# Optimization experiments

Measured on AMD Instinct MI355X. Metric: run time of the kernel, lower is better.

The kernel has to match this reference:

```python
import jax, jax.numpy as jnp
import numpy as np

GROUP_SIZE = 128  # vLLM machete default group size
ZERO_POINT = 8.0  # uint4b8: stored unsigned 4-bit, logical value = q - 8


def setup_inputs() -> dict:
    key = jax.random.key(0)
    k_a, k_b, k_s = jax.random.split(key, 3)
    M, K, N = 4096, 4096, 12288
    a = jax.random.normal(k_a, (M, K), dtype=jnp.float32)
    # int4 quantized weights stored as small ints in [0, 16)
    b_q = jax.random.randint(k_b, (K, N), 0, 16, dtype=jnp.int32)
    # per-group scales: one scale per (group of 128 rows of K) per output column
    scales = jax.random.uniform(k_s, (K // GROUP_SIZE, N), dtype=jnp.float32) * 0.02 + 0.001
    return {"a": a, "b_q": b_q, "scales": scales}


def reference(a, b_q, scales):
    K, N = b_q.shape
    G = K // GROUP_SIZE
    # dequantize: (q - 8) * group_scale, scale broadcast over each K-group
    b = (b_q.astype(jnp.float32) - ZERO_POINT).reshape(G, GROUP_SIZE, N)
    b = (b * scales[:, None, :]).reshape(K, N)  # [K, N] dequantized weights
    return a @ b  # [M, N]
```

## Files before the change

kernel.cpp:

```cpp
#include <hip/hip_runtime.h>
#include <hip/hip_bf16.h>
#include <stdint.h>

constexpr int Mdim = 4096;
constexpr int Kdim = 4096;
constexpr int Ndim = 12288;

constexpr int NKT = Kdim / 64;
constexpr int GM = Mdim / 256;
constexpr int GN = Ndim / 128;
constexpr int NWGP = GM * GN;
constexpr int GRID_M = Mdim / 128;
constexpr int GRID_N = Ndim / 128;
constexpr int NWG = GRID_M * GRID_N;

typedef float  f32x4   __attribute__((ext_vector_type(4)));
typedef __bf16 bf16x4v __attribute__((ext_vector_type(4)));
typedef __bf16 bf16x8v __attribute__((ext_vector_type(8)));
typedef int    i32x4   __attribute__((ext_vector_type(4)));
typedef unsigned short ushort8 __attribute__((ext_vector_type(8)));

typedef __attribute__((address_space(3))) uint32_t       lds_u32;
typedef __attribute__((address_space(1))) const uint32_t glb_u32;

__device__ __forceinline__ void gload16(const void* g, void* l) {
    __builtin_amdgcn_global_load_lds((glb_u32*)(uintptr_t)g,
                                     (lds_u32*)(uint32_t)(uintptr_t)l, 16, 0, 0);
}


__launch_bounds__(256)
__global__ void cvtA(const float* __restrict__ A, unsigned short* __restrict__ Aw) {
    int t = blockIdx.x * 256 + threadIdx.x;
    int r = t >> 9;
    int c = t & 511;
    const float* src = A + ((long)r << 12) + (c << 3);
    f32x4 v0 = *(const f32x4*)src;
    f32x4 v1 = *(const f32x4*)(src + 4);
    bf16x8v o;
#pragma unroll
    for (int j = 0; j < 4; ++j) { o[j] = (__bf16)v0[j]; o[4 + j] = (__bf16)v1[j]; }
    int ks = c & 3;
    int cp = (c & ~3) | (ks ^ ((r >> 1) & 3));
    *(bf16x8v*)(Aw + ((long)r << 12) + (cp << 3)) = o;
}

__launch_bounds__(256)
__global__ void deqB(const int* __restrict__ Bq, const float* __restrict__ S,
                     unsigned short* __restrict__ Bw) {
    __shared__ unsigned short lt[64][72];
    int kb = blockIdx.x & 63;
    int nb = blockIdx.x >> 6;
    int k0 = kb << 6, n0 = nb << 6;
    int tid = threadIdx.x;
    int g = k0 >> 7;
    int nq = (tid & 15) << 2;
    f32x4 sc = *(const f32x4*)(S + (long)g * Ndim + n0 + nq);
#pragma unroll
    for (int p = 0; p < 4; ++p) {
        int kk = (p << 4) + (tid >> 4);
        i32x4 q = *(const i32x4*)(Bq + (long)(k0 + kk) * Ndim + n0 + nq);
#pragma unroll
        for (int j = 0; j < 4; ++j) {
            float v = ((float)q[j] - 8.f) * sc[j];
            lt[nq + j][kk] = __builtin_bit_cast(unsigned short, (__bf16)v);
        }
    }
    __syncthreads();
#pragma unroll
    for (int h = 0; h < 2; ++h) {
        int cidx = tid + (h << 8);
        int n = cidx >> 3, sidx = cidx & 7;
        int kh = sidx >> 2, ks = sidx & 3;
        int ksp = ks ^ ((n >> 1) & 3);
        ushort8 v = *(const ushort8*)&lt[n][sidx << 3];
        *(ushort8*)(Bw + (long)(n0 + n) * Kdim + k0 + kh * 32 + ksp * 8) = v;
    }
}

__launch_bounds__(256, 2)
__global__ void gemm_p(const unsigned short* __restrict__ Aw,
                       const unsigned short* __restrict__ Bw,
                       float* __restrict__ C) {
    extern __shared__ unsigned char lds[];

    const int tid  = threadIdx.x;
    const int lane = tid & 63;
    const int w    = tid >> 6;
    const int wr   = w >> 1, wc = w & 1;
    const int fr   = lane & 15;
    const int ks   = lane >> 4;

    const int bid = blockIdx.x;
    const int xcd = bid & 7;
    const int loc = bid >> 3;
    const int pn  = loc >> 4;
    const int tm  = loc & 15;
    const int tn  = xcd * 12 + pn;
    const int brow = tm << 8, bcol = tn << 7;

    const unsigned char* pa0 = (const unsigned char*)Aw
        + (size_t)(brow + (tid >> 2)) * 8192 + (size_t)(tid & 3) * 16;
    const unsigned char* pa1 = pa0 + (size_t)64 * 8192;
    const unsigned char* pa2 = pa0 + (size_t)128 * 8192;
    const unsigned char* pa3 = pa0 + (size_t)192 * 8192;
    const unsigned char* pb0 = (const unsigned char*)Bw
        + (size_t)(bcol + (tid >> 2)) * 8192 + (size_t)(tid & 3) * 16;
    const unsigned char* pb1 = pb0 + (size_t)64 * 8192;
    const int ldw = w << 10;

    int offA[8], offB[4];
#pragma unroll
    for (int m = 0; m < 8; ++m) {
        int rA = wr * 128 + m * 16 + fr;
        offA[m] = rA * 64 + ((ks ^ ((rA >> 1) & 3)) << 4);
    }
#pragma unroll
    for (int n = 0; n < 4; ++n) {
        int cB = wc * 64 + n * 16 + fr;
        offB[n] = 16384 + cB * 64 + ((ks ^ ((cB >> 1) & 3)) << 4);
    }

    f32x4 acc[8][4];
#pragma unroll
    for (int m = 0; m < 8; ++m)
#pragma unroll
        for (int n = 0; n < 4; ++n) acc[m][n] = (f32x4){0.f, 0.f, 0.f, 0.f};

#define STAGEA(R, OFF)                                                        \
    gload16(pa0 + (OFF), lds + (R) * 24576 + 0 * 4096 + ldw);                 \
    gload16(pa1 + (OFF), lds + (R) * 24576 + 1 * 4096 + ldw);                 \
    gload16(pa2 + (OFF), lds + (R) * 24576 + 2 * 4096 + ldw);                 \
    gload16(pa3 + (OFF), lds + (R) * 24576 + 3 * 4096 + ldw);
#define STAGEB(R, OFF)                                                        \
    gload16(pb0 + (OFF), lds + (R) * 24576 + 16384 + 0 * 4096 + ldw);         \
    gload16(pb1 + (OFF), lds + (R) * 24576 + 16384 + 1 * 4096 + ldw);

#define RD(R, off) (*(const bf16x8v*)(lds + (R) * 24576 + (off)))

#define HSTEP(R, J, STG, VM)                                                  \
    {                                                                         \
        bf16x8v a[8], b[4];                                                   \
        _Pragma("unroll") for (int m = 0; m < 4; ++m) a[m] = RD(R, offA[m]);  \
        _Pragma("unroll") for (int n = 0; n < 4; ++n) b[n] = RD(R, offB[n]);  \
        if (STG) { STAGEA(((R) + 2) % 3, ((J) + 2) * 64) }                    \
        __builtin_amdgcn_s_barrier();                                         \
        __builtin_amdgcn_s_setprio(1);                                        \
        _Pragma("unroll") for (int m = 0; m < 4; ++m)                         \
            _Pragma("unroll") for (int n = 0; n < 4; ++n)                     \
                acc[m][n] = __builtin_amdgcn_mfma_f32_16x16x32_bf16(          \
                    a[m], b[n], acc[m][n], 0, 0, 0);                          \
        __builtin_amdgcn_s_setprio(0);                                        \
        __builtin_amdgcn_s_barrier();                                         \
        _Pragma("unroll") for (int m = 4; m < 8; ++m) a[m] = RD(R, offA[m]);  \
        if (STG) { STAGEB(((R) + 2) % 3, ((J) + 2) * 64) }                    \
        __builtin_amdgcn_s_barrier();                                         \
        __builtin_amdgcn_s_setprio(1);                                        \
        _Pragma("unroll") for (int m = 4; m < 8; ++m)                         \
            _Pragma("unroll") for (int n = 0; n < 4; ++n)                     \
                acc[m][n] = __builtin_amdgcn_mfma_f32_16x16x32_bf16(          \
                    a[m], b[n], acc[m][n], 0, 0, 0);                          \
        __builtin_amdgcn_s_setprio(0);                                        \
        asm volatile("s_waitcnt vmcnt(" #VM ")" ::: "memory");                \
        __builtin_amdgcn_s_barrier();                                         \
    }

    STAGEA(0, 0) STAGEB(0, 0)
    STAGEA(1, 64) STAGEB(1, 64)
    asm volatile("s_waitcnt vmcnt(6)" ::: "memory");
    __builtin_amdgcn_s_barrier();

    for (int it = 0; it < 42; ++it) {
        HSTEP(0, 0, 1, 6)
        HSTEP(1, 1, 1, 6)
        HSTEP(2, 2, 1, 6)
        pa0 += 192; pa1 += 192; pa2 += 192; pa3 += 192;
        pb0 += 192; pb1 += 192;
    }
    HSTEP(0, 0, 0, 0)
    {
        bf16x8v a[8], b[4];
#pragma unroll
        for (int m = 0; m < 8; ++m) a[m] = RD(1, offA[m]);
#pragma unroll
        for (int n = 0; n < 4; ++n) b[n] = RD(1, offB[n]);
#pragma unroll
        for (int m = 0; m < 8; ++m)
#pragma unroll
            for (int n = 0; n < 4; ++n)
                acc[m][n] = __builtin_amdgcn_mfma_f32_16x16x32_bf16(
                    a[m], b[n], acc[m][n], 0, 0, 0);
    }

#pragma unroll
    for (int m = 0; m < 8; ++m) {
        int row = brow + wr * 128 + m * 16 + ks * 4;
#pragma unroll
        for (int n = 0; n < 4; ++n) {
            int col = bcol + wc * 64 + n * 16 + fr;
            f32x4 v = acc[m][n];
            float* cp = C + (size_t)row * Ndim + col;
#pragma unroll
            for (int r = 0; r < 4; ++r) cp[(size_t)r * Ndim] = v[r];
        }
    }
#undef HSTEP
#undef RD
#undef STAGEB
#undef STAGEA
}

__launch_bounds__(256, 3)
__global__ void gemm_bf16(const unsigned short* __restrict__ Aw,
                          const unsigned short* __restrict__ Bw,
                          float* __restrict__ C) {
    __shared__ unsigned char sA[128 * 64 * 2];
    __shared__ unsigned char sB[128 * 64 * 2];

    const int tid  = threadIdx.x;
    const int lane = tid & 63;
    const int w    = tid >> 6;

    const int bid   = blockIdx.x;
    const int x     = bid & 7;
    const int local = bid >> 3;
    const int pn    = local >> 5;
    const int tm    = local & 31;
    const int tn    = x * 12 + pn;
    const int brow  = tm << 7;
    const int bcol  = tn << 7;

    const unsigned char* ga[4];
    const unsigned char* gb[4];
#pragma unroll
    for (int i = 0; i < 4; ++i) {
        int c = (w << 8) + (i << 6) + lane;
        int r = c >> 3, s = c & 7;
        ga[i] = (const unsigned char*)Aw + (long)(brow + r) * 8192 + (s << 4);
        gb[i] = (const unsigned char*)Bw + (long)(bcol + r) * 8192 + (s << 4);
    }

    const int fr = lane & 15;
    const int ks = lane >> 4;
    const int wr = w >> 1, wc = w & 1;
    int ra[4][2], rb[4][2];
#pragma unroll
    for (int m = 0; m < 4; ++m)
#pragma unroll
        for (int kk = 0; kk < 2; ++kk) {
            int r_a = wr * 64 + m * 16 + fr;
            int r_b = wc * 64 + m * 16 + fr;
            ra[m][kk] = (r_a << 7) + (kk << 6) + ((ks ^ ((r_a >> 1) & 3)) << 4);
            rb[m][kk] = (r_b << 7) + (kk << 6) + ((ks ^ ((r_b >> 1) & 3)) << 4);
        }

    f32x4 acc[4][4];
#pragma unroll
    for (int m = 0; m < 4; ++m)
#pragma unroll
        for (int n = 0; n < 4; ++n) acc[m][n] = (f32x4){0.f, 0.f, 0.f, 0.f};

    for (int kt = 0; kt < NKT; ++kt) {
#pragma unroll
        for (int i = 0; i < 4; ++i) {
            gload16(ga[i], sA + (((w << 2) + i) << 10));
            gload16(gb[i], sB + (((w << 2) + i) << 10));
            ga[i] += 128;
            gb[i] += 128;
        }
        __syncthreads();

#pragma unroll
        for (int kk = 0; kk < 2; ++kk) {
            bf16x8v af[4], bf[4];
#pragma unroll
            for (int m = 0; m < 4; ++m) af[m] = *(const bf16x8v*)(sA + ra[m][kk]);
#pragma unroll
            for (int n = 0; n < 4; ++n) bf[n] = *(const bf16x8v*)(sB + rb[n][kk]);
#pragma unroll
            for (int m = 0; m < 4; ++m)
#pragma unroll
                for (int n = 0; n < 4; ++n)
                    acc[m][n] = __builtin_amdgcn_mfma_f32_16x16x32_bf16(af[m], bf[n], acc[m][n], 0, 0, 0);
        }
        __syncthreads();
    }

#pragma unroll
    for (int m = 0; m < 4; ++m) {
        int row = brow + wr * 64 + m * 16 + ks * 4;
#pragma unroll
        for (int n = 0; n < 4; ++n) {
            int col = bcol + wc * 64 + n * 16 + fr;
            f32x4 v = acc[m][n];
            float* cp = C + (long)row * Ndim + col;
#pragma unroll
            for (int r = 0; r < 4; ++r) cp[(long)r * Ndim] = v[r];
        }
    }
}

__device__ __forceinline__ int swz_f(int row, int kbyte) {
    int s = kbyte >> 4;
    int f = s ^ ((row ^ (row >> 2)) & 7);
    return (row << 7) + (f << 4) + (kbyte & 15);
}

__launch_bounds__(256, 2)
__global__ void machete_fused(const float* __restrict__ A,
                              const int* __restrict__ Bq,
                              const float* __restrict__ S,
                              float* __restrict__ C) {
    __shared__ unsigned char sA[128 * 64 * 2];
    __shared__ unsigned char sB[128 * 64 * 2];

    const int tid = threadIdx.x;
    const int bid = blockIdx.x;
    const int sid = (bid & 7) * (NWG / 8) + (bid >> 3);
    const int tm = sid / GRID_N;
    const int tn = sid % GRID_N;
    const int brow = tm * 128;
    const int bcol = tn * 128;

    const int a_row0 = tid >> 4;
    const int a_kb   = tid & 15;
    const int b_kb = tid >> 4;
    const int b_nb = tid & 15;

    int aw[8];
#pragma unroll
    for (int i = 0; i < 8; ++i) aw[i] = swz_f(a_row0 + 16 * i, a_kb * 8);
    int bw[2][4];
#pragma unroll
    for (int i = 0; i < 2; ++i)
#pragma unroll
        for (int j = 0; j < 4; ++j) bw[i][j] = swz_f(4 * b_nb + 64 * i + j, b_kb * 8);

    const int lane = tid & 63;
    const int w  = tid >> 6;
    const int wr = w >> 1, wc = w & 1;
    const int fr = lane & 15;
    const int ks = lane >> 4;
    int ar[4][2], br[4][2];
#pragma unroll
    for (int m = 0; m < 4; ++m)
#pragma unroll
        for (int kk = 0; kk < 2; ++kk) {
            ar[m][kk] = swz_f(wr * 64 + m * 16 + fr, kk * 64 + ks * 16);
            br[m][kk] = swz_f(wc * 64 + m * 16 + fr, kk * 64 + ks * 16);
        }

    const float* Ap = A + (long)brow * Kdim;
    const int*   Bp = Bq + bcol;

    f32x4 aregs[8];
    i32x4 bregs[2][4];
    f32x4 sregs[2];

#pragma unroll
    for (int i = 0; i < 8; ++i)
        aregs[i] = *(const f32x4*)(Ap + (long)(a_row0 + 16 * i) * Kdim + a_kb * 4);
#pragma unroll
    for (int i = 0; i < 2; ++i) {
#pragma unroll
        for (int r = 0; r < 4; ++r)
            bregs[i][r] = *(const i32x4*)(Bp + (long)(b_kb * 4 + r) * Ndim + 4 * b_nb + 64 * i);
        sregs[i] = *(const f32x4*)(S + bcol + 4 * b_nb + 64 * i);
    }

    f32x4 acc[4][4];
#pragma unroll
    for (int m = 0; m < 4; ++m)
#pragma unroll
        for (int n = 0; n < 4; ++n) acc[m][n] = (f32x4){0.f, 0.f, 0.f, 0.f};

    for (int kt = 0; kt < NKT; ++kt) {
#pragma unroll
        for (int i = 0; i < 8; ++i) {
            f32x4 v = aregs[i];
            bf16x4v p;
            p[0] = (__bf16)v[0]; p[1] = (__bf16)v[1];
            p[2] = (__bf16)v[2]; p[3] = (__bf16)v[3];
            *(bf16x4v*)(sA + aw[i]) = p;
        }
#pragma unroll
        for (int i = 0; i < 2; ++i) {
            f32x4 sc = sregs[i];
#pragma unroll
            for (int j = 0; j < 4; ++j) {
                float scj = sc[j];
                float nm8 = -8.f * scj;
                bf16x4v p;
#pragma unroll
                for (int r = 0; r < 4; ++r) {
                    float v = (float)bregs[i][r][j] * scj + nm8;
                    p[r] = (__bf16)v;
                }
                *(bf16x4v*)(sB + bw[i][j]) = p;
            }
        }
        __syncthreads();

        if (kt + 1 < NKT) {
            const float* Ap2 = Ap + (kt + 1) * 64;
            const int*   Bp2 = Bq + bcol + (long)((kt + 1) * 64) * Ndim;
            const float* Sp2 = S + (long)((kt + 1) >> 1) * Ndim + bcol;
#pragma unroll
            for (int i = 0; i < 8; ++i)
                aregs[i] = *(const f32x4*)(Ap2 + (long)(a_row0 + 16 * i) * Kdim + a_kb * 4);
#pragma unroll
            for (int i = 0; i < 2; ++i) {
#pragma unroll
                for (int r = 0; r < 4; ++r)
                    bregs[i][r] = *(const i32x4*)(Bp2 + (long)(b_kb * 4 + r) * Ndim + 4 * b_nb + 64 * i);
                sregs[i] = *(const f32x4*)(Sp2 + 4 * b_nb + 64 * i);
            }
        }

#pragma unroll
        for (int kk = 0; kk < 2; ++kk) {
            bf16x8v af[4], bfv[4];
#pragma unroll
            for (int m = 0; m < 4; ++m) af[m] = *(const bf16x8v*)(sA + ar[m][kk]);
#pragma unroll
            for (int n = 0; n < 4; ++n) bfv[n] = *(const bf16x8v*)(sB + br[n][kk]);
#pragma unroll
            for (int m = 0; m < 4; ++m)
#pragma unroll
                for (int n = 0; n < 4; ++n)
                    acc[m][n] = __builtin_amdgcn_mfma_f32_16x16x32_bf16(af[m], bfv[n], acc[m][n], 0, 0, 0);
        }
        __syncthreads();
    }

#pragma unroll
    for (int m = 0; m < 4; ++m) {
        int row = brow + wr * 64 + m * 16 + ks * 4;
#pragma unroll
        for (int n = 0; n < 4; ++n) {
            int col = bcol + wc * 64 + n * 16 + fr;
            f32x4 v = acc[m][n];
            float* cp = C + (long)row * Ndim + col;
#pragma unroll
            for (int r = 0; r < 4; ++r) cp[(long)r * Ndim] = v[r];
        }
    }
}

extern "C" void kernel_launch(void* const* d_in, const int* in_sizes, int n_in,
                              void* d_out, int out_size, void* d_ws, size_t ws_size,
                              hipStream_t stream) {
    const float* A  = (const float*)d_in[0];
    const int*   Bq = (const int*)d_in[1];
    const float* S  = (const float*)d_in[2];
    float* C = (float*)d_out;

    const size_t a_elems = (size_t)Mdim * Kdim;
    const size_t b_elems = (size_t)Ndim * Kdim;
    const size_t need = (a_elems + b_elems) * sizeof(unsigned short);

    if (ws_size >= need) {
        unsigned short* Aw = (unsigned short*)d_ws;
        unsigned short* Bw = Aw + a_elems;
        hipLaunchKernelGGL(cvtA, dim3((Mdim * Kdim / 8) / 256), dim3(256), 0, stream, A, Aw);
        hipLaunchKernelGGL(deqB, dim3((Kdim / 64) * (Ndim / 64)), dim3(256), 0, stream, Bq, S, Bw);
        hipError_t e = hipFuncSetAttribute(
            reinterpret_cast<const void*>(gemm_p),
            hipFuncAttributeMaxDynamicSharedMemorySize, 73728);
        if (e == hipSuccess) {
            hipLaunchKernelGGL(gemm_p, dim3(NWGP), dim3(256), 73728, stream, Aw, Bw, C);
        } else {
            hipLaunchKernelGGL(gemm_bf16, dim3(NWG), dim3(256), 0, stream, Aw, Bw, C);
        }
    } else {
        hipLaunchKernelGGL(machete_fused, dim3(NWG), dim3(256), 0, stream, A, Bq, S, C);
    }
}
```

Baseline: 517.5 us.

## Switch main GEMM to 256x256 tiles with 512 threads and double-buffered 128-K stages

Replaces the 256x128, 256-thread GEMM with a 256x256 output tile computed by 8 waves (2x4). Each stage loads 128 K, split into two 64-wide halves, into a double-buffered 128 KB LDS layout, and global loads for the next halves are issued between the MFMA blocks. The larger tile raises arithmetic intensity per byte loaded and halves B traffic per output. In exchange it uses far more LDS, so likely only one workgroup fits per CU, and the larger grid tiles may leave the device less evenly filled.

Result: faster. 468.3 us (-9.5%).

```diff
diff --git a/kernel.cpp b/kernel.cpp
--- a/kernel.cpp
+++ b/kernel.cpp
@@ -7,9 +7,9 @@
 constexpr int Ndim = 12288;
 
 constexpr int NKT = Kdim / 64;
-constexpr int GM = Mdim / 256;
-constexpr int GN = Ndim / 128;
-constexpr int NWGP = GM * GN;
+constexpr int GM256 = Mdim / 256;
+constexpr int GN256 = Ndim / 256;
+constexpr int NWG256 = GM256 * GN256;
 constexpr int GRID_M = Mdim / 128;
 constexpr int GRID_N = Ndim / 128;
 constexpr int NWG = GRID_M * GRID_N;
@@ -78,16 +78,16 @@
     }
 }
 
-__launch_bounds__(256, 2)
-__global__ void gemm_p(const unsigned short* __restrict__ Aw,
-                       const unsigned short* __restrict__ Bw,
-                       float* __restrict__ C) {
-    extern __shared__ unsigned char lds[];
+__launch_bounds__(512, 2)
+__global__ void gemm256(const unsigned short* __restrict__ Aw,
+                        const unsigned short* __restrict__ Bw,
+                        float* __restrict__ C) {
+    extern __shared__ unsigned char ldsbuf[];
 
     const int tid  = threadIdx.x;
     const int lane = tid & 63;
     const int w    = tid >> 6;
-    const int wr   = w >> 1, wc = w & 1;
+    const int wr   = w >> 2, wc = w & 3;
     const int fr   = lane & 15;
     const int ks   = lane >> 4;
 
@@ -96,30 +96,32 @@
     const int loc = bid >> 3;
     const int pn  = loc >> 4;
     const int tm  = loc & 15;
-    const int tn  = xcd * 12 + pn;
-    const int brow = tm << 8, bcol = tn << 7;
-
-    const unsigned char* pa0 = (const unsigned char*)Aw
+    const int tn  = xcd * 6 + pn;
+    const int brow = tm << 8, bcol = tn << 8;
+
+    const unsigned char* pA = (const unsigned char*)Aw
         + (size_t)(brow + (tid >> 2)) * 8192 + (size_t)(tid & 3) * 16;
-    const unsigned char* pa1 = pa0 + (size_t)64 * 8192;
-    const unsigned char* pa2 = pa0 + (size_t)128 * 8192;
-    const unsigned char* pa3 = pa0 + (size_t)192 * 8192;
-    const unsigned char* pb0 = (const unsigned char*)Bw
+    const unsigned char* pA2 = pA + (size_t)128 * 8192;
+    const unsigned char* pB = (const unsigned char*)Bw
         + (size_t)(bcol + (tid >> 2)) * 8192 + (size_t)(tid & 3) * 16;
-    const unsigned char* pb1 = pb0 + (size_t)64 * 8192;
+    const unsigned char* pB2 = pB + (size_t)128 * 8192;
     const int ldw = w << 10;
 
-    int offA[8], offB[4];
-#pragma unroll
-    for (int m = 0; m < 8; ++m) {
-        int rA = wr * 128 + m * 16 + fr;
-        offA[m] = rA * 64 + ((ks ^ ((rA >> 1) & 3)) << 4);
-    }
-#pragma unroll
-    for (int n = 0; n < 4; ++n) {
-        int cB = wc * 64 + n * 16 + fr;
-        offB[n] = 16384 + cB * 64 + ((ks ^ ((cB >> 1) & 3)) << 4);
-    }
+    int offA[8][2], offB[4][2];
+#pragma unroll
+    for (int am = 0; am < 8; ++am)
+#pragma unroll
+        for (int kh = 0; kh < 2; ++kh) {
+            int rowL = wr * 128 + am * 16 + fr;
+            offA[am][kh] = (kh << 14) + rowL * 64 + ((ks ^ ((rowL >> 1) & 3)) << 4);
+        }
+#pragma unroll
+    for (int n = 0; n < 4; ++n)
+#pragma unroll
+        for (int kh = 0; kh < 2; ++kh) {
+            int colL = wc * 64 + n * 16 + fr;
+            offB[n][kh] = (kh << 14) + colL * 64 + ((ks ^ ((colL >> 1) & 3)) << 4);
+        }
 
     f32x4 acc[8][4];
 #pragma unroll
@@ -127,69 +129,77 @@
 #pragma unroll
         for (int n = 0; n < 4; ++n) acc[m][n] = (f32x4){0.f, 0.f, 0.f, 0.f};
 
-#define STAGEA(R, OFF)                                                        \
-    gload16(pa0 + (OFF), lds + (R) * 24576 + 0 * 4096 + ldw);                 \
-    gload16(pa1 + (OFF), lds + (R) * 24576 + 1 * 4096 + ldw);                 \
-    gload16(pa2 + (OFF), lds + (R) * 24576 + 2 * 4096 + ldw);                 \
-    gload16(pa3 + (OFF), lds + (R) * 24576 + 3 * 4096 + ldw);
-#define STAGEB(R, OFF)                                                        \
-    gload16(pb0 + (OFF), lds + (R) * 24576 + 16384 + 0 * 4096 + ldw);         \
-    gload16(pb1 + (OFF), lds + (R) * 24576 + 16384 + 1 * 4096 + ldw);
-
-#define RD(R, off) (*(const bf16x8v*)(lds + (R) * 24576 + (off)))
-
-#define HSTEP(R, J, STG, VM)                                                  \
+#define STG_A(DSTB, OFF)                                                      \
+    gload16(pA  + (OFF), ldsbuf + (DSTB) + ldw);                              \
+    gload16(pA2 + (OFF), ldsbuf + (DSTB) + ldw + 8192);
+#define STG_B(DSTB, OFF)                                                      \
+    gload16(pB  + (OFF), ldsbuf + (DSTB) + 32768 + ldw);                      \
+    gload16(pB2 + (OFF), ldsbuf + (DSTB) + 32768 + ldw + 8192);
+
+#define TILE(BUF, O1, O2, STG1, STG2, VM)                                     \
     {                                                                         \
-        bf16x8v a[8], b[4];                                                   \
-        _Pragma("unroll") for (int m = 0; m < 4; ++m) a[m] = RD(R, offA[m]);  \
-        _Pragma("unroll") for (int n = 0; n < 4; ++n) b[n] = RD(R, offB[n]);  \
-        if (STG) { STAGEA(((R) + 2) % 3, ((J) + 2) * 64) }                    \
-        __builtin_amdgcn_s_barrier();                                         \
+        unsigned char* sAc = ldsbuf + ((BUF) << 16);                          \
+        unsigned char* sBc = sAc + 32768;                                     \
+        bf16x8v aF[8], bF[4];                                                 \
+        _Pragma("unroll") for (int m = 0; m < 8; ++m)                         \
+            aF[m] = *(const bf16x8v*)(sAc + offA[m][0]);                      \
+        _Pragma("unroll") for (int n = 0; n < 4; ++n)                         \
+            bF[n] = *(const bf16x8v*)(sBc + offB[n][0]);                      \
+        if (STG1) { STG_A(((1 - (BUF)) << 16) + (1 << 14), O1)                \
+                    STG_B(((1 - (BUF)) << 16) + (1 << 14), O1) }              \
         __builtin_amdgcn_s_setprio(1);                                        \
-        _Pragma("unroll") for (int m = 0; m < 4; ++m)                         \
+        _Pragma("unroll") for (int m = 0; m < 8; ++m)                         \
             _Pragma("unroll") for (int n = 0; n < 4; ++n)                     \
                 acc[m][n] = __builtin_amdgcn_mfma_f32_16x16x32_bf16(          \
-                    a[m], b[n], acc[m][n], 0, 0, 0);                          \
+                    aF[m], bF[n], acc[m][n], 0, 0, 0);                        \
         __builtin_amdgcn_s_setprio(0);                                        \
         __builtin_amdgcn_s_barrier();                                         \
-        _Pragma("unroll") for (int m = 4; m < 8; ++m) a[m] = RD(R, offA[m]);  \
-        if (STG) { STAGEB(((R) + 2) % 3, ((J) + 2) * 64) }                    \
-        __builtin_amdgcn_s_barrier();                                         \
+        __builtin_amdgcn_sched_barrier(0);   \
+        _Pragma("unroll") for (int m = 0; m < 8; ++m)                         \
+            aF[m] = *(const bf16x8v*)(sAc + offA[m][1]);                      \
+        _Pragma("unroll") for (int n = 0; n < 4; ++n)                         \
+            bF[n] = *(const bf16x8v*)(sBc + offB[n][1]);                      \
+        if (STG2) { STG_A(((BUF) << 16), O2)                                  \
+                    STG_B(((BUF) << 16), O2) }                                \
         __builtin_amdgcn_s_setprio(1);                                        \
-        _Pragma("unroll") for (int m = 4; m < 8; ++m)                         \
+        _Pragma("unroll") for (int m = 0; m < 8; ++m)                         \
             _Pragma("unroll") for (int n = 0; n < 4; ++n)                     \
                 acc[m][n] = __builtin_amdgcn_mfma_f32_16x16x32_bf16(          \
-                    a[m], b[n], acc[m][n], 0, 0, 0);                          \
+                    aF[m], bF[n], acc[m][n], 0, 0, 0);                        \
         __builtin_amdgcn_s_setprio(0);                                        \
         asm volatile("s_waitcnt vmcnt(" #VM ")" ::: "memory");                \
         __builtin_amdgcn_s_barrier();                                         \
     }
 
-    STAGEA(0, 0) STAGEB(0, 0)
-    STAGEA(1, 64) STAGEB(1, 64)
-    asm volatile("s_waitcnt vmcnt(6)" ::: "memory");
+    STG_A(0, 0)                 STG_B(0, 0)
+    STG_A((1 << 14), 64)        STG_B((1 << 14), 64)
+    STG_A((1 << 16), 128)       STG_B((1 << 16), 128)
+    asm volatile("s_waitcnt vmcnt(4)" ::: "memory");
     __builtin_amdgcn_s_barrier();
 
-    for (int it = 0; it < 42; ++it) {
-        HSTEP(0, 0, 1, 6)
-        HSTEP(1, 1, 1, 6)
-        HSTEP(2, 2, 1, 6)
-        pa0 += 192; pa1 += 192; pa2 += 192; pa3 += 192;
-        pb0 += 192; pb1 += 192;
-    }
-    HSTEP(0, 0, 0, 0)
+    for (int it = 0; it < 31; ++it) {
+        TILE(0, 192, 256, 1, 1, 4)
+        TILE(1, 320, 384, 1, 1, 4)
+        pA += 256; pA2 += 256; pB += 256; pB2 += 256;
+    }
+    TILE(0, 192, 0, 1, 0, 0)
     {
-        bf16x8v a[8], b[4];
-#pragma unroll
-        for (int m = 0; m < 8; ++m) a[m] = RD(1, offA[m]);
-#pragma unroll
-        for (int n = 0; n < 4; ++n) b[n] = RD(1, offB[n]);
-#pragma unroll
-        for (int m = 0; m < 8; ++m)
-#pragma unroll
-            for (int n = 0; n < 4; ++n)
-                acc[m][n] = __builtin_amdgcn_mfma_f32_16x16x32_bf16(
-                    a[m], b[n], acc[m][n], 0, 0, 0);
+        unsigned char* sAc = ldsbuf + (1 << 16);
+        unsigned char* sBc = sAc + 32768;
+#pragma unroll
+        for (int kh = 0; kh < 2; ++kh) {
+            bf16x8v aF[8], bF[4];
+#pragma unroll
+            for (int m = 0; m < 8; ++m) aF[m] = *(const bf16x8v*)(sAc + offA[m][kh]);
+#pragma unroll
+            for (int n = 0; n < 4; ++n) bF[n] = *(const bf16x8v*)(sBc + offB[n][kh]);
+#pragma unroll
+            for (int m = 0; m < 8; ++m)
+#pragma unroll
+                for (int n = 0; n < 4; ++n)
+                    acc[m][n] = __builtin_amdgcn_mfma_f32_16x16x32_bf16(
+                        aF[m], bF[n], acc[m][n], 0, 0, 0);
+        }
     }
 
 #pragma unroll
@@ -204,10 +214,9 @@
             for (int r = 0; r < 4; ++r) cp[(size_t)r * Ndim] = v[r];
         }
     }
-#undef HSTEP
-#undef RD
-#undef STAGEB
-#undef STAGEA
+#undef TILE
+#undef STG_B
+#undef STG_A
 }
 
 __launch_bounds__(256, 3)
@@ -465,10 +474,10 @@
         hipLaunchKernelGGL(cvtA, dim3((Mdim * Kdim / 8) / 256), dim3(256), 0, stream, A, Aw);
         hipLaunchKernelGGL(deqB, dim3((Kdim / 64) * (Ndim / 64)), dim3(256), 0, stream, Bq, S, Bw);
         hipError_t e = hipFuncSetAttribute(
-            reinterpret_cast<const void*>(gemm_p),
-            hipFuncAttributeMaxDynamicSharedMemorySize, 73728);
+            reinterpret_cast<const void*>(gemm256),
+            hipFuncAttributeMaxDynamicSharedMemorySize, 131072);
         if (e == hipSuccess) {
-            hipLaunchKernelGGL(gemm_p, dim3(NWGP), dim3(256), 73728, stream, Aw, Bw, C);
+            hipLaunchKernelGGL(gemm256, dim3(NWG256), dim3(512), 131072, stream, Aw, Bw, C);
         } else {
             hipLaunchKernelGGL(gemm_bf16, dim3(NWG), dim3(256), 0, stream, Aw, Bw, C);
         }
```
